# Optimization experiments

Measured on AMD Instinct MI355X. Metric: run time of the kernel, lower is better.

The kernel has to match this reference:

```python
import jax, jax.numpy as jnp
import numpy as np

B, S, D = 4, 2048, 1024
H = 16
HD = D // H  # 64


def setup_inputs() -> dict:
    key = jax.random.key(0)
    ks = jax.random.split(key, 9)
    sc = 1.0 / np.sqrt(D)
    return {
        "hidden_states": jax.random.normal(ks[0], (B, S, D), jnp.float32),
        "Wq": jax.random.normal(ks[1], (D, D), jnp.float32) * sc,
        "bq": jnp.zeros((D,), jnp.float32),
        "Wk": jax.random.normal(ks[2], (D, D), jnp.float32) * sc,
        "bk": jnp.zeros((D,), jnp.float32),
        "Wv": jax.random.normal(ks[3], (D, D), jnp.float32) * sc,
        "bv": jnp.zeros((D,), jnp.float32),
        "Wo": jax.random.normal(ks[4], (D, D), jnp.float32) * sc,
        "bo": jnp.zeros((D,), jnp.float32),
    }


def _rope_emb(seq_len, head_dim, dtype):
    # Faithful to torch buffer: emb = cat(sin(pos*inv_freq), cos(pos*inv_freq))
    inv_freq = 1.0 / (10000.0 ** (jnp.arange(0, head_dim, 2, dtype=jnp.float32) / head_dim))
    sinusoid = jnp.arange(seq_len, dtype=jnp.float32)[:, None] * inv_freq[None, :]  # [S, hd/2]
    return jnp.concatenate([jnp.sin(sinusoid), jnp.cos(sinusoid)], axis=-1).astype(dtype)  # [S, hd]


def _rotate(x, c, s):
    # x: [B,H,S,hd]; c,s: [1,1,S,hd/2]
    x1, x2 = x[..., : HD // 2], x[..., HD // 2 :]
    return jnp.concatenate([x1 * c - x2 * s, x2 * c + x1 * s], axis=-1)


def reference(hidden_states, Wq, bq, Wk, bk, Wv, bv, Wo, bo):
    b, s, d = hidden_states.shape

    def proj(W, bias):
        y = jnp.einsum("bsd,ed->bse", hidden_states, W) + bias
        return y.reshape(b, s, H, HD).transpose(0, 2, 1, 3)  # [B,H,S,hd]

    q, k, v = proj(Wq, bq), proj(Wk, bk), proj(Wv, bv)

    emb = _rope_emb(s, HD, hidden_states.dtype)
    # NOTE: original code names first half 'cos' though the buffer stores sin first.
    c = emb[None, None, :, : HD // 2]
    sn = emb[None, None, :, HD // 2 :]
    q = _rotate(q, c, sn)
    k = _rotate(k, c, sn)

    scores = jnp.einsum("bhqd,bhkd->bhqk", q, k) / jnp.sqrt(jnp.asarray(HD, hidden_states.dtype))
    probs = jax.nn.softmax(scores, axis=-1)
    ctx = jnp.einsum("bhqk,bhkd->bhqd", probs, v)
    ctx = ctx.transpose(0, 2, 1, 3).reshape(b, s, d)  # [B,S,D]
    return jnp.einsum("bsd,ed->bse", ctx, Wo) + bo
```

## Files before the change

### kernel.cpp

```cpp
#include <hip/hip_runtime.h>
#include <cmath>

#define B_ 4
#define S_ 2048
#define D_ 1024
#define H_ 16
#define HD_ 64

typedef __attribute__((ext_vector_type(8))) _Float16 half8;
typedef __attribute__((ext_vector_type(2))) _Float16 half2t;
typedef __attribute__((ext_vector_type(2))) __fp16 fp16x2;
typedef __attribute__((ext_vector_type(4))) float floatx4;
typedef __attribute__((ext_vector_type(16))) float floatx16;
typedef __attribute__((ext_vector_type(2))) unsigned uint2v;

union H2U { unsigned u; half2t h; fp16x2 f; };
__device__ __forceinline__ unsigned hpack2(float a, float b) {
    H2U x; x.h[0] = (_Float16)a; x.h[1] = (_Float16)b; return x.u;
}
__device__ __forceinline__ unsigned pkrtz(float a, float b) {
    H2U x; x.f = __builtin_amdgcn_cvt_pkrtz(a, b); return x.u;
}
__device__ __forceinline__ float h_lo(unsigned u) { H2U x; x.u = u; return (float)x.h[0]; }
__device__ __forceinline__ float h_hi(unsigned u) { H2U x; x.u = u; return (float)x.h[1]; }

__device__ __forceinline__ void barrier_lgkm() {
    asm volatile("s_waitcnt lgkmcnt(0)\n\ts_barrier" ::: "memory");
}

__global__ __launch_bounds__(256)
void conv_x(const float* __restrict__ x, unsigned short* __restrict__ o, int n)
{
    const int i = (blockIdx.x * 256 + threadIdx.x) * 8;
    if (i >= n) return;
    const float4 a = *(const float4*)(x + i);
    const float4 b = *(const float4*)(x + i + 4);
    *(uint4*)(o + i) = make_uint4(hpack2(a.x, a.y), hpack2(a.z, a.w),
                                  hpack2(b.x, b.y), hpack2(b.z, b.w));
}

__global__ __launch_bounds__(256)
void conv_weights(const float* __restrict__ Wq, const float* __restrict__ Wk,
                  const float* __restrict__ Wv, const float* __restrict__ Wo,
                  const float* __restrict__ bq, const float* __restrict__ bk,
                  const float* __restrict__ bv,
                  unsigned short* __restrict__ Wqkvf, unsigned short* __restrict__ Wof,
                  float* __restrict__ bqkv)
{
    const int bxx = blockIdx.x;
    const int t = threadIdx.x;
    if (bxx < 2048) {
        const int w = bxx >> 9;
        const int i = ((bxx & 511) * 256 + t) * 8;
        const float* src = (w == 0) ? Wq : (w == 1) ? Wk : (w == 2) ? Wv : Wo;
        const float4 a = *(const float4*)(src + i);
        const float4 b = *(const float4*)(src + i + 4);
        const uint4 v = make_uint4(hpack2(a.x, a.y), hpack2(a.z, a.w),
                                   hpack2(b.x, b.y), hpack2(b.z, b.w));
        if (w < 3)
            *(uint4*)(Wqkvf + (size_t)w * 1048576 + i) = v;
        else
            *(uint4*)(Wof + i) = v;
    } else {
        const int idx = t * 4;
        *(float4*)(bqkv + idx)        = *(const float4*)(bq + idx);
        *(float4*)(bqkv + 1024 + idx) = *(const float4*)(bk + idx);
        *(float4*)(bqkv + 2048 + idx) = *(const float4*)(bv + idx);
    }
}

template<int OBF>
__global__ __launch_bounds__(256, 2)
void gemm_half(const unsigned short* __restrict__ Ap, const unsigned short* __restrict__ Bp,
               const float* __restrict__ bias, void* __restrict__ Cout,
               int M, int N, int K)
{
    __shared__ uint4 ASH[512];
    __shared__ uint4 BSH[512];

    const int tid = threadIdx.x;
    const int bm = blockIdx.x * 128;
    const int bn = blockIdx.y * 128;
    const int w = tid >> 6, l = tid & 63;
    const int wm = (w & 1) * 64, wn = (w >> 1) * 64;

    floatx4 acc[4][4];
#pragma unroll
    for (int i = 0; i < 4; ++i)
#pragma unroll
        for (int j = 0; j < 4; ++j)
#pragma unroll
            for (int r = 0; r < 4; ++r) acc[i][j][r] = 0.f;

    const int r0 = tid >> 1, scb = (tid & 1) * 2;
    const size_t ga = (size_t)(bm + r0) * K + scb * 8;
    const size_t gb = (size_t)(bn + r0) * K + scb * 8;
    const int blk = r0 >> 4, r15 = r0 & 15;
    const int p1 = (scb << 4) + r15;
    const int f0a = (blk << 6) + (p1 ^ (scb << 1));
    const int f0b = (blk << 6) + ((p1 + 16) ^ ((scb + 1) << 1));

    const half8* pA = (const half8*)ASH;
    const half8* pB = (const half8*)BSH;
    const int lg = l ^ ((l >> 4) << 1);
    const int am = (wm >> 4) * 64 + lg;
    const int bnf = (wn >> 4) * 64 + lg;

    uint4 vA0 = *(const uint4*)(Ap + ga);
    uint4 vA1 = *(const uint4*)(Ap + ga + 8);
    uint4 vB0 = *(const uint4*)(Bp + gb);
    uint4 vB1 = *(const uint4*)(Bp + gb + 8);

    for (int k0 = 0; k0 < K; k0 += 32) {
        __syncthreads();
        ASH[f0a] = vA0; ASH[f0b] = vA1;
        BSH[f0a] = vB0; BSH[f0b] = vB1;
        __syncthreads();

        const int kn = (k0 + 32 < K) ? k0 + 32 : k0;
        vA0 = *(const uint4*)(Ap + ga + kn);
        vA1 = *(const uint4*)(Ap + ga + kn + 8);
        vB0 = *(const uint4*)(Bp + gb + kn);
        vB1 = *(const uint4*)(Bp + gb + kn + 8);

        half8 a[4];
#pragma unroll
        for (int i = 0; i < 4; ++i) a[i] = pA[am + i * 64];
#pragma unroll
        for (int j = 0; j < 4; ++j) {
            const half8 b = pB[bnf + j * 64];
#pragma unroll
            for (int i = 0; i < 4; ++i)
                acc[i][j] = __builtin_amdgcn_mfma_f32_16x16x32_f16(a[i], b, acc[i][j], 0, 0, 0);
        }
    }

    const int cr = (l >> 4) << 2;
    const int cc = l & 15;
#pragma unroll
    for (int j = 0; j < 4; ++j) {
        const int col = bn + wn + j * 16 + cc;
        const float bv = bias[col];
#pragma unroll
        for (int i = 0; i < 4; ++i) {
            const int row = bm + wm + i * 16 + cr;
#pragma unroll
            for (int r = 0; r < 4; ++r) {
                const float vv = acc[i][j][r] + bv;
                if (OBF) {
                    ((unsigned short*)Cout)[(size_t)(row + r) * N + col] =
                        (unsigned short)(hpack2(vv, vv) & 0xffffu);
                } else {
                    ((float*)Cout)[(size_t)(row + r) * N + col] = vv;
                }
            }
        }
    }
}

__global__ __launch_bounds__(256)
void prep_fused(const unsigned short* __restrict__ qkv,
                unsigned short* __restrict__ Qf, unsigned short* __restrict__ Kfo,
                unsigned short* __restrict__ Vt)
{
    __shared__ unsigned T[64][65];
    const int bx = blockIdx.x;
    const int t = threadIdx.x;
    if (bx < B_ * S_) {
        const int s = bx & (S_ - 1);
        const size_t rbase = (size_t)bx * 3072;
        const size_t obase = (size_t)bx * D_;
        const int h = t >> 4;
        const int i2 = (t & 15) * 2;
        const float kfreq = 0.28782313662425572f;
        const float KS = 0.18033688011112042f;

        const float f0 = expf(-(float)i2 * kfreq);
        const float f1 = expf(-(float)(i2 + 1) * kfreq);
        const float t0 = (float)s * f0, t1 = (float)s * f1;
        const float sn0 = sinf(t0), cs0 = cosf(t0);
        const float sn1 = sinf(t1), cs1 = cosf(t1);

        const size_t c1 = (size_t)h * 64 + i2;
        const size_t c2 = c1 + 32;

        const unsigned uq1 = *(const unsigned*)(qkv + rbase + c1);
        const unsigned uq2 = *(const unsigned*)(qkv + rbase + c2);
        const unsigned uk1 = *(const unsigned*)(qkv + rbase + 1024 + c1);
        const unsigned uk2 = *(const unsigned*)(qkv + rbase + 1024 + c2);
        const float q1x = h_lo(uq1), q1y = h_hi(uq1);
        const float q2x = h_lo(uq2), q2y = h_hi(uq2);
        const float k1x = h_lo(uk1), k1y = h_hi(uk1);
        const float k2x = h_lo(uk2), k2y = h_hi(uk2);

        *(unsigned*)(Qf + obase + c1) = hpack2(q1x * sn0 - q2x * cs0, q1y * sn1 - q2y * cs1);
        *(unsigned*)(Qf + obase + c2) = hpack2(q2x * sn0 + q1x * cs0, q2y * sn1 + q1y * cs1);
        *(unsigned*)(Kfo + obase + c1) = hpack2((k1x * sn0 - k2x * cs0) * KS, (k1y * sn1 - k2y * cs1) * KS);
        *(unsigned*)(Kfo + obase + c2) = hpack2((k2x * sn0 + k1x * cs0) * KS, (k2y * sn1 + k1y * cs1) * KS);
    } else {
        const int vb = bx - B_ * S_;
        const int st = vb & 31;
        const int h  = (vb >> 5) & 15;
        const int b  = vb >> 9;
        const int s0 = st * 64;
#pragma unroll
        for (int it = 0; it < 2; ++it) {
            const int idx = it * 256 + t;
            const int row = idx >> 3;
            const int c8 = (idx & 7) * 8;
            const uint4 u = *(const uint4*)(qkv + ((size_t)(b * S_ + s0 + row)) * 3072 + 2048 + h * 64 + c8);
            T[row][c8+0] = u.x & 0xffffu; T[row][c8+1] = u.x >> 16;
            T[row][c8+2] = u.y & 0xffffu; T[row][c8+3] = u.y >> 16;
            T[row][c8+4] = u.z & 0xffffu; T[row][c8+5] = u.z >> 16;
            T[row][c8+6] = u.w & 0xffffu; T[row][c8+7] = u.w >> 16;
        }
        __syncthreads();
        const int d = t >> 2;
        const int scg = (t & 3) * 16;
        unsigned u[8];
#pragma unroll
        for (int ii = 0; ii < 8; ++ii)
            u[ii] = T[scg + 2*ii][d] | (T[scg + 2*ii + 1][d] << 16);
        unsigned short* dst = Vt + ((size_t)((b * H_ + h) * 64 + d)) * S_ + s0 + scg;
        *(uint4*)(dst)     = make_uint4(u[0], u[1], u[2], u[3]);
        *(uint4*)(dst + 8) = make_uint4(u[4], u[5], u[6], u[7]);
    }
}

__global__ __launch_bounds__(256)
void attn_mfma32(const unsigned short* __restrict__ Qf,
                 const unsigned short* __restrict__ Kfi,
                 const unsigned short* __restrict__ Vt,
                 unsigned short* __restrict__ Cf)
{
    __shared__ uint4 KF[2][512];
    __shared__ uint4 VF[2][512];

    const int t = threadIdx.x;
    const int i = blockIdx.x;
    const int xcd = i & 7, j = i >> 3;
    const int bh = xcd * 8 + (j >> 4);
    const int qblk = j & 15;
    const int b = bh >> 4, h = bh & 15;

    const int w = t >> 6, l = t & 63;
    const int lq = l & 31, h5 = l >> 5;
    const int qrow = qblk * 128 + w * 32 + lq;

    half8 qf[4];
    const unsigned short* qp = Qf + ((size_t)(b * S_ + qrow)) * D_ + h * 64 + h5 * 8;
#pragma unroll
    for (int kc = 0; kc < 4; ++kc) qf[kc] = *(const half8*)(qp + kc * 16);

    floatx16 o0, o1, o2, z16;
#pragma unroll
    for (int r = 0; r < 16; ++r) { o0[r] = 0.f; o1[r] = 0.f; o2[r] = 0.f; z16[r] = 0.f; }

    union { unsigned u[4]; half8 s; } onesf;
    const unsigned ov = (lq == 0) ? 0x3C003C00u : 0u;
    onesf.u[0] = ov; onesf.u[1] = ov; onesf.u[2] = ov; onesf.u[3] = ov;

    const int sr = t >> 2, sc = t & 3;
    const unsigned short* gK0 = Kfi + ((size_t)(b * S_ + sr)) * D_ + h * 64 + sc * 16;
    const unsigned short* gV0 = Vt + ((size_t)((b * H_ + h) * 64 + sr)) * S_ + sc * 16;
    const int e0 = (sr >> 5) * 256 + sc * 64 + ((sr & 31) ^ (sc << 1));
    const int lx[4] = { l, l ^ 2, l ^ 4, l ^ 6 };

    const half8* pK = (const half8*)KF;
    const half8* pV = (const half8*)VF;
    (void)pK; (void)pV;

    uint4 ka  = *(const uint4*)(gK0);
    uint4 kb2 = *(const uint4*)(gK0 + 8);
    uint4 va  = *(const uint4*)(gV0);
    uint4 vb2 = *(const uint4*)(gV0 + 8);
    KF[0][e0] = ka; KF[0][e0 + 32] = kb2;
    VF[0][e0] = va; VF[0][e0 + 32] = vb2;
    {
        const unsigned short* gK = gK0 + (size_t)64 * D_;
        const unsigned short* gV = gV0 + 64;
        ka  = *(const uint4*)(gK);
        kb2 = *(const uint4*)(gK + 8);
        va  = *(const uint4*)(gV);
        vb2 = *(const uint4*)(gV + 8);
    }
    __syncthreads();

    for (int kt = 0; kt < 32; ++kt) {
        const int cur = kt & 1;

        if (kt < 31) {
            uint4* wK = KF[cur ^ 1];
            uint4* wV = VF[cur ^ 1];
            wK[e0] = ka; wK[e0 + 32] = kb2;
            wV[e0] = va; wV[e0 + 32] = vb2;
        }
        if (kt < 30) {
            const unsigned short* gK = gK0 + (size_t)(kt + 2) * 64 * D_;
            const unsigned short* gV = gV0 + (size_t)(kt + 2) * 64;
            ka  = *(const uint4*)(gK);
            kb2 = *(const uint4*)(gK + 8);
            va  = *(const uint4*)(gV);
            vb2 = *(const uint4*)(gV + 8);
        }

        const half8* pKc = (const half8*)KF[cur];
        const half8* pVc = (const half8*)VF[cur];

        __builtin_amdgcn_s_setprio(1);
        floatx16 st0 = __builtin_amdgcn_mfma_f32_32x32x16_f16(pKc[lx[0]],           qf[0], z16, 0, 0, 0);
        floatx16 st1 = __builtin_amdgcn_mfma_f32_32x32x16_f16(pKc[4 * 64 + lx[0]],  qf[0], z16, 0, 0, 0);
#pragma unroll
        for (int kc = 1; kc < 4; ++kc) {
            st0 = __builtin_amdgcn_mfma_f32_32x32x16_f16(pKc[kc * 64 + lx[kc]],       qf[kc], st0, 0, 0, 0);
            st1 = __builtin_amdgcn_mfma_f32_32x32x16_f16(pKc[(4 + kc) * 64 + lx[kc]], qf[kc], st1, 0, 0, 0);
        }
        __builtin_amdgcn_s_setprio(0);

        unsigned pu0[8], pu1[8];
#pragma unroll
        for (int g = 0; g < 8; ++g) {
            pu0[g] = pkrtz(__builtin_amdgcn_exp2f(st0[2 * g]),
                           __builtin_amdgcn_exp2f(st0[2 * g + 1]));
            pu1[g] = pkrtz(__builtin_amdgcn_exp2f(st1[2 * g]),
                           __builtin_amdgcn_exp2f(st1[2 * g + 1]));
        }

        __builtin_amdgcn_s_setprio(1);
#pragma unroll
        for (int kc = 0; kc < 4; ++kc) {
            const unsigned* pus = (kc >> 1) ? pu1 : pu0;
            const int g0 = (kc & 1) * 4;
            const uint2v r02 = __builtin_amdgcn_permlane32_swap(pus[g0 + 0], pus[g0 + 2], false, false);
            const uint2v r13 = __builtin_amdgcn_permlane32_swap(pus[g0 + 1], pus[g0 + 3], false, false);
            union { unsigned u[4]; half8 s; } pf;
            pf.u[0] = r02[0];
            pf.u[1] = r13[0];
            pf.u[2] = r02[1];
            pf.u[3] = r13[1];
            o0 = __builtin_amdgcn_mfma_f32_32x32x16_f16(pVc[kc * 64 + lx[kc]],       pf.s, o0, 0, 0, 0);
            o1 = __builtin_amdgcn_mfma_f32_32x32x16_f16(pVc[(4 + kc) * 64 + lx[kc]], pf.s, o1, 0, 0, 0);
            o2 = __builtin_amdgcn_mfma_f32_32x32x16_f16(onesf.s,                     pf.s, o2, 0, 0, 0);
        }
        __builtin_amdgcn_s_setprio(0);

        if (kt < 31) barrier_lgkm();
    }

    union { float f; unsigned u; } lc; lc.f = o2[0];
    const uint2v lr = __builtin_amdgcn_permlane32_swap(lc.u, lc.u, false, false);
    union { unsigned u; float f; } ls; ls.u = lr[0];
    const float inv = 1.0f / ls.f;

    const size_t cbase = ((size_t)(b * S_ + qrow)) * D_ + h * 64;
#pragma unroll
    for (int rq = 0; rq < 4; ++rq) {
        const int d0 = rq * 8 + h5 * 4;
        const uint2 y0 = make_uint2(hpack2(o0[4*rq+0] * inv, o0[4*rq+1] * inv),
                                    hpack2(o0[4*rq+2] * inv, o0[4*rq+3] * inv));
        const uint2 y1 = make_uint2(hpack2(o1[4*rq+0] * inv, o1[4*rq+1] * inv),
                                    hpack2(o1[4*rq+2] * inv, o1[4*rq+3] * inv));
        *(uint2*)(Cf + cbase + d0)      = y0;
        *(uint2*)(Cf + cbase + 32 + d0) = y1;
    }
}

extern "C" void kernel_launch(void* const* d_in, const int* in_sizes, int n_in,
                              void* d_out, int out_size, void* d_ws, size_t ws_size,
                              hipStream_t stream) {
    (void)in_sizes; (void)n_in; (void)out_size; (void)ws_size;
    const float* X  = (const float*)d_in[0];
    const float* Wq = (const float*)d_in[1];
    const float* bq = (const float*)d_in[2];
    const float* Wk = (const float*)d_in[3];
    const float* bk = (const float*)d_in[4];
    const float* Wv = (const float*)d_in[5];
    const float* bv = (const float*)d_in[6];
    const float* Wo = (const float*)d_in[7];
    const float* bo = (const float*)d_in[8];
    float* out = (float*)d_out;

    char* ws = (char*)d_ws;
#define OFF(mb) (ws + ((size_t)(mb) << 20))
    unsigned short* Xf    = (unsigned short*)OFF(0);
    unsigned short* qkv16 = (unsigned short*)OFF(16);
    unsigned short* Qf    = (unsigned short*)OFF(64);
    unsigned short* Kfb   = (unsigned short*)OFF(80);
    unsigned short* Vtb   = (unsigned short*)OFF(96);
    unsigned short* Wqkvf = (unsigned short*)OFF(112);
    unsigned short* Wof   = (unsigned short*)OFF(118);
    float*          bqkv  = (float*)OFF(120);
    unsigned short* Cf    = (unsigned short*)OFF(0);
#undef OFF

    const int NX = B_ * S_ * D_;
    conv_x<<<NX / 2048, 256, 0, stream>>>(X, Xf, NX);
    conv_weights<<<2049, 256, 0, stream>>>(Wq, Wk, Wv, Wo, bq, bk, bv,
                                           Wqkvf, Wof, bqkv);
    gemm_half<1><<<dim3(64, 24), 256, 0, stream>>>(Xf, Wqkvf, bqkv,
                                                   qkv16, B_*S_, 3 * D_, D_);
    prep_fused<<<B_*S_ + 2048, 256, 0, stream>>>(qkv16, Qf, Kfb, Vtb);
    attn_mfma32<<<1024, 256, 0, stream>>>(Qf, Kfb, Vtb, Cf);
    gemm_half<0><<<dim3(64, 8), 256, 0, stream>>>(Cf, Wof, bo, out, B_*S_, D_, D_);
}
```

Measured before the change: 306.6 us.

## Software-pipeline PV MFMAs one tile behind QK and triple-buffer V

Restructures the attention loop so the P·V MFMAs for tile kt-1 run after the QK and exp work of tile kt, which lets the exp/convert phase overlap with matrix work. V shared memory goes from double to triple buffering to hold the lagging tile, and a drain step handles the last tile after the loop. It also adds a launch-bounds occupancy hint of 4 blocks per CU. The costs are more registers for the carried P fragments, more LDS, and possible spilling under the new launch bound.

```diff
diff --git a/kernel.cpp b/kernel.cpp
--- a/kernel.cpp
+++ b/kernel.cpp
@@ -227,14 +227,14 @@
     }
 }
 
-__global__ __launch_bounds__(256)
+__global__ __launch_bounds__(256, 4)
 void attn_mfma32(const unsigned short* __restrict__ Qf,
                  const unsigned short* __restrict__ Kfi,
                  const unsigned short* __restrict__ Vt,
                  unsigned short* __restrict__ Cf)
 {
     __shared__ uint4 KF[2][512];
-    __shared__ uint4 VF[2][512];
+    __shared__ uint4 VF[3][512];
 
     const int t = threadIdx.x;
     const int i = blockIdx.x;
@@ -265,10 +265,6 @@
     const unsigned short* gV0 = Vt + ((size_t)((b * H_ + h) * 64 + sr)) * S_ + sc * 16;
     const int e0 = (sr >> 5) * 256 + sc * 64 + ((sr & 31) ^ (sc << 1));
     const int lx[4] = { l, l ^ 2, l ^ 4, l ^ 6 };
-
-    const half8* pK = (const half8*)KF;
-    const half8* pV = (const half8*)VF;
-    (void)pK; (void)pV;
 
     uint4 ka  = *(const uint4*)(gK0);
     uint4 kb2 = *(const uint4*)(gK0 + 8);
@@ -286,12 +282,13 @@
     }
     __syncthreads();
 
+    unsigned pfr[4][4];
+    int vm1 = 2, vcur = 0, vp1 = 1;
+
     for (int kt = 0; kt < 32; ++kt) {
-        const int cur = kt & 1;
-
         if (kt < 31) {
-            uint4* wK = KF[cur ^ 1];
-            uint4* wV = VF[cur ^ 1];
+            uint4* wK = KF[(kt + 1) & 1];
+            uint4* wV = VF[vp1];
             wK[e0] = ka; wK[e0 + 32] = kb2;
             wV[e0] = va; wV[e0 + 32] = vb2;
         }
@@ -304,8 +301,7 @@
             vb2 = *(const uint4*)(gV + 8);
         }
 
-        const half8* pKc = (const half8*)KF[cur];
-        const half8* pVc = (const half8*)VF[cur];
+        const half8* pKc = (const half8*)KF[kt & 1];
 
         __builtin_amdgcn_s_setprio(1);
         floatx16 st0 = __builtin_amdgcn_mfma_f32_32x32x16_f16(pKc[lx[0]],           qf[0], z16, 0, 0, 0);
@@ -326,25 +322,49 @@
                            __builtin_amdgcn_exp2f(st1[2 * g + 1]));
         }
 
-        __builtin_amdgcn_s_setprio(1);
+        if (kt > 0) {
+            const half8* pVc = (const half8*)VF[vm1];
+            __builtin_amdgcn_s_setprio(1);
+#pragma unroll
+            for (int kc = 0; kc < 4; ++kc) {
+                union { unsigned u[4]; half8 s; } pfs;
+                pfs.u[0] = pfr[kc][0]; pfs.u[1] = pfr[kc][1];
+                pfs.u[2] = pfr[kc][2]; pfs.u[3] = pfr[kc][3];
+                o0 = __builtin_amdgcn_mfma_f32_32x32x16_f16(pVc[kc * 64 + lx[kc]],       pfs.s, o0, 0, 0, 0);
+                o1 = __builtin_amdgcn_mfma_f32_32x32x16_f16(pVc[(4 + kc) * 64 + lx[kc]], pfs.s, o1, 0, 0, 0);
+                o2 = __builtin_amdgcn_mfma_f32_32x32x16_f16(onesf.s,                     pfs.s, o2, 0, 0, 0);
+            }
+            __builtin_amdgcn_s_setprio(0);
+        }
+
 #pragma unroll
         for (int kc = 0; kc < 4; ++kc) {
             const unsigned* pus = (kc >> 1) ? pu1 : pu0;
             const int g0 = (kc & 1) * 4;
             const uint2v r02 = __builtin_amdgcn_permlane32_swap(pus[g0 + 0], pus[g0 + 2], false, false);
             const uint2v r13 = __builtin_amdgcn_permlane32_swap(pus[g0 + 1], pus[g0 + 3], false, false);
-            union { unsigned u[4]; half8 s; } pf;
-            pf.u[0] = r02[0];
-            pf.u[1] = r13[0];
-            pf.u[2] = r02[1];
-            pf.u[3] = r13[1];
-            o0 = __builtin_amdgcn_mfma_f32_32x32x16_f16(pVc[kc * 64 + lx[kc]],       pf.s, o0, 0, 0, 0);
-            o1 = __builtin_amdgcn_mfma_f32_32x32x16_f16(pVc[(4 + kc) * 64 + lx[kc]], pf.s, o1, 0, 0, 0);
-            o2 = __builtin_amdgcn_mfma_f32_32x32x16_f16(onesf.s,                     pf.s, o2, 0, 0, 0);
-        }
-        __builtin_amdgcn_s_setprio(0);
+            pfr[kc][0] = r02[0];
+            pfr[kc][1] = r13[0];
+            pfr[kc][2] = r02[1];
+            pfr[kc][3] = r13[1];
+        }
+
+        { const int tmp = vm1; vm1 = vcur; vcur = vp1; vp1 = tmp; }
 
         if (kt < 31) barrier_lgkm();
+    }
+
+    {
+        const half8* pVc = (const half8*)VF[vm1];
+#pragma unroll
+        for (int kc = 0; kc < 4; ++kc) {
+            union { unsigned u[4]; half8 s; } pfs;
+            pfs.u[0] = pfr[kc][0]; pfs.u[1] = pfr[kc][1];
+            pfs.u[2] = pfr[kc][2]; pfs.u[3] = pfr[kc][3];
+            o0 = __builtin_amdgcn_mfma_f32_32x32x16_f16(pVc[kc * 64 + lx[kc]],       pfs.s, o0, 0, 0, 0);
+            o1 = __builtin_amdgcn_mfma_f32_32x32x16_f16(pVc[(4 + kc) * 64 + lx[kc]], pfs.s, o1, 0, 0, 0);
+            o2 = __builtin_amdgcn_mfma_f32_32x32x16_f16(onesf.s,                     pfs.s, o2, 0, 0, 0);
+        }
     }
 
     union { float f; unsigned u; } lc; lc.f = o2[0];
```

Measured after the change: 405.3 us. +32.2%, slower.

## Fuse RoPE into QKV GEMM epilogue and merge conversion kernels

Applied to the files above, without the earlier changes.

The QKV projection GEMM now applies the rotary embedding and the K scaling in its epilogue and writes Q and K straight to their final buffers. Only V goes to a temporary buffer, which a smaller transpose kernel then reads. The input and weight fp32-to-fp16 conversion kernels are merged into one launch. This drops the full qkv intermediate round trip and one launch, but the epilogue now computes sin/cos per element, which adds transcendental work inside the GEMM.

```diff
diff --git a/kernel.cpp b/kernel.cpp
--- a/kernel.cpp
+++ b/kernel.cpp
@@ -29,26 +29,25 @@
 }
 
 __global__ __launch_bounds__(256)
-void conv_x(const float* __restrict__ x, unsigned short* __restrict__ o, int n)
+void conv_all(const float* __restrict__ x, unsigned short* __restrict__ o,
+              const float* __restrict__ Wq, const float* __restrict__ Wk,
+              const float* __restrict__ Wv, const float* __restrict__ Wo,
+              const float* __restrict__ bq, const float* __restrict__ bk,
+              const float* __restrict__ bv,
+              unsigned short* __restrict__ Wqkvf, unsigned short* __restrict__ Wof,
+              float* __restrict__ bqkv)
 {
-    const int i = (blockIdx.x * 256 + threadIdx.x) * 8;
-    if (i >= n) return;
-    const float4 a = *(const float4*)(x + i);
-    const float4 b = *(const float4*)(x + i + 4);
-    *(uint4*)(o + i) = make_uint4(hpack2(a.x, a.y), hpack2(a.z, a.w),
-                                  hpack2(b.x, b.y), hpack2(b.z, b.w));
-}
-
-__global__ __launch_bounds__(256)
-void conv_weights(const float* __restrict__ Wq, const float* __restrict__ Wk,
-                  const float* __restrict__ Wv, const float* __restrict__ Wo,
-                  const float* __restrict__ bq, const float* __restrict__ bk,
-                  const float* __restrict__ bv,
-                  unsigned short* __restrict__ Wqkvf, unsigned short* __restrict__ Wof,
-                  float* __restrict__ bqkv)
-{
-    const int bxx = blockIdx.x;
     const int t = threadIdx.x;
+    const int bx = blockIdx.x;
+    if (bx < 4096) {
+        const int i = (bx * 256 + t) * 8;
+        const float4 a = *(const float4*)(x + i);
+        const float4 b = *(const float4*)(x + i + 4);
+        *(uint4*)(o + i) = make_uint4(hpack2(a.x, a.y), hpack2(a.z, a.w),
+                                      hpack2(b.x, b.y), hpack2(b.z, b.w));
+        return;
+    }
+    const int bxx = bx - 4096;
     if (bxx < 2048) {
         const int w = bxx >> 9;
         const int i = ((bxx & 511) * 256 + t) * 8;
@@ -69,10 +68,11 @@
     }
 }
 
-template<int OBF>
+template<int MODE>
 __global__ __launch_bounds__(256, 2)
 void gemm_half(const unsigned short* __restrict__ Ap, const unsigned short* __restrict__ Bp,
-               const float* __restrict__ bias, void* __restrict__ Cout,
+               const float* __restrict__ bias, void* __restrict__ C0,
+               void* __restrict__ C1, void* __restrict__ C2,
                int M, int N, int K)
 {
     __shared__ uint4 ASH[512];
@@ -137,94 +137,105 @@
 
     const int cr = (l >> 4) << 2;
     const int cc = l & 15;
-#pragma unroll
-    for (int j = 0; j < 4; ++j) {
-        const int col = bn + wn + j * 16 + cc;
-        const float bv = bias[col];
-#pragma unroll
-        for (int i = 0; i < 4; ++i) {
-            const int row = bm + wm + i * 16 + cr;
-#pragma unroll
-            for (int r = 0; r < 4; ++r) {
-                const float vv = acc[i][j][r] + bv;
-                if (OBF) {
-                    ((unsigned short*)Cout)[(size_t)(row + r) * N + col] =
-                        (unsigned short)(hpack2(vv, vv) & 0xffffu);
-                } else {
-                    ((float*)Cout)[(size_t)(row + r) * N + col] = vv;
+
+    if (MODE == 0) {
+#pragma unroll
+        for (int j = 0; j < 4; ++j) {
+            const int col = bn + wn + j * 16 + cc;
+            const float bv = bias[col];
+#pragma unroll
+            for (int i = 0; i < 4; ++i) {
+                const int row = bm + wm + i * 16 + cr;
+#pragma unroll
+                for (int r = 0; r < 4; ++r) {
+                    ((float*)C0)[(size_t)(row + r) * N + col] = acc[i][j][r] + bv;
                 }
             }
         }
+    } else {
+        const int reg = bn >> 10;
+        if (reg < 2) {
+            const float KSs = (reg == 1) ? 0.18033688011112042f : 1.0f;
+            unsigned short* dst0 = (unsigned short*)((reg == 0) ? C0 : C1);
+            const int hbase = (bn - (reg << 10)) + wn;
+            const float kfreq = 0.28782313662425572f;
+#pragma unroll
+            for (int j = 0; j < 2; ++j) {
+                const int d = j * 16 + cc;
+                const float fd = expf(-(float)d * kfreq);
+                const float b1 = bias[bn + wn + j * 16 + cc];
+                const float b2 = bias[bn + wn + j * 16 + cc + 32];
+#pragma unroll
+                for (int i = 0; i < 4; ++i) {
+                    const int row0 = bm + wm + i * 16 + cr;
+#pragma unroll
+                    for (int r = 0; r < 4; ++r) {
+                        const int row = row0 + r;
+                        const int s = row & (S_ - 1);
+                        const float tt = (float)s * fd;
+                        const float sn = sinf(tt), cs = cosf(tt);
+                        const float x1 = acc[i][j][r] + b1;
+                        const float x2 = acc[i][j + 2][r] + b2;
+                        const float o1 = (x1 * sn - x2 * cs) * KSs;
+                        const float o2 = (x2 * sn + x1 * cs) * KSs;
+                        unsigned short* p = dst0 + (size_t)row * D_ + hbase + d;
+                        p[0]  = (unsigned short)(hpack2(o1, o1) & 0xffffu);
+                        p[32] = (unsigned short)(hpack2(o2, o2) & 0xffffu);
+                    }
+                }
+            }
+        } else {
+#pragma unroll
+            for (int j = 0; j < 4; ++j) {
+                const int col = bn + wn + j * 16 + cc;
+                const float bv = bias[col];
+                const int vcol = col - 2048;
+#pragma unroll
+                for (int i = 0; i < 4; ++i) {
+                    const int row0 = bm + wm + i * 16 + cr;
+#pragma unroll
+                    for (int r = 0; r < 4; ++r) {
+                        const float vv = acc[i][j][r] + bv;
+                        ((unsigned short*)C2)[(size_t)(row0 + r) * 1024 + vcol] =
+                            (unsigned short)(hpack2(vv, vv) & 0xffffu);
+                    }
+                }
+            }
+        }
     }
 }
 
 __global__ __launch_bounds__(256)
-void prep_fused(const unsigned short* __restrict__ qkv,
-                unsigned short* __restrict__ Qf, unsigned short* __restrict__ Kfo,
-                unsigned short* __restrict__ Vt)
+void prep_v(const unsigned short* __restrict__ Vtmp, unsigned short* __restrict__ Vt)
 {
     __shared__ unsigned T[64][65];
-    const int bx = blockIdx.x;
+    const int vb = blockIdx.x;
     const int t = threadIdx.x;
-    if (bx < B_ * S_) {
-        const int s = bx & (S_ - 1);
-        const size_t rbase = (size_t)bx * 3072;
-        const size_t obase = (size_t)bx * D_;
-        const int h = t >> 4;
-        const int i2 = (t & 15) * 2;
-        const float kfreq = 0.28782313662425572f;
-        const float KS = 0.18033688011112042f;
-
-        const float f0 = expf(-(float)i2 * kfreq);
-        const float f1 = expf(-(float)(i2 + 1) * kfreq);
-        const float t0 = (float)s * f0, t1 = (float)s * f1;
-        const float sn0 = sinf(t0), cs0 = cosf(t0);
-        const float sn1 = sinf(t1), cs1 = cosf(t1);
-
-        const size_t c1 = (size_t)h * 64 + i2;
-        const size_t c2 = c1 + 32;
-
-        const unsigned uq1 = *(const unsigned*)(qkv + rbase + c1);
-        const unsigned uq2 = *(const unsigned*)(qkv + rbase + c2);
-        const unsigned uk1 = *(const unsigned*)(qkv + rbase + 1024 + c1);
-        const unsigned uk2 = *(const unsigned*)(qkv + rbase + 1024 + c2);
-        const float q1x = h_lo(uq1), q1y = h_hi(uq1);
-        const float q2x = h_lo(uq2), q2y = h_hi(uq2);
-        const float k1x = h_lo(uk1), k1y = h_hi(uk1);
-        const float k2x = h_lo(uk2), k2y = h_hi(uk2);
-
-        *(unsigned*)(Qf + obase + c1) = hpack2(q1x * sn0 - q2x * cs0, q1y * sn1 - q2y * cs1);
-        *(unsigned*)(Qf + obase + c2) = hpack2(q2x * sn0 + q1x * cs0, q2y * sn1 + q1y * cs1);
-        *(unsigned*)(Kfo + obase + c1) = hpack2((k1x * sn0 - k2x * cs0) * KS, (k1y * sn1 - k2y * cs1) * KS);
-        *(unsigned*)(Kfo + obase + c2) = hpack2((k2x * sn0 + k1x * cs0) * KS, (k2y * sn1 + k1y * cs1) * KS);
-    } else {
-        const int vb = bx - B_ * S_;
-        const int st = vb & 31;
-        const int h  = (vb >> 5) & 15;
-        const int b  = vb >> 9;
-        const int s0 = st * 64;
-#pragma unroll
-        for (int it = 0; it < 2; ++it) {
-            const int idx = it * 256 + t;
-            const int row = idx >> 3;
-            const int c8 = (idx & 7) * 8;
-            const uint4 u = *(const uint4*)(qkv + ((size_t)(b * S_ + s0 + row)) * 3072 + 2048 + h * 64 + c8);
-            T[row][c8+0] = u.x & 0xffffu; T[row][c8+1] = u.x >> 16;
-            T[row][c8+2] = u.y & 0xffffu; T[row][c8+3] = u.y >> 16;
-            T[row][c8+4] = u.z & 0xffffu; T[row][c8+5] = u.z >> 16;
-            T[row][c8+6] = u.w & 0xffffu; T[row][c8+7] = u.w >> 16;
-        }
-        __syncthreads();
-        const int d = t >> 2;
-        const int scg = (t & 3) * 16;
-        unsigned u[8];
-#pragma unroll
-        for (int ii = 0; ii < 8; ++ii)
-            u[ii] = T[scg + 2*ii][d] | (T[scg + 2*ii + 1][d] << 16);
-        unsigned short* dst = Vt + ((size_t)((b * H_ + h) * 64 + d)) * S_ + s0 + scg;
-        *(uint4*)(dst)     = make_uint4(u[0], u[1], u[2], u[3]);
-        *(uint4*)(dst + 8) = make_uint4(u[4], u[5], u[6], u[7]);
-    }
+    const int st = vb & 31;
+    const int h  = (vb >> 5) & 15;
+    const int b  = vb >> 9;
+    const int s0 = st * 64;
+#pragma unroll
+    for (int it = 0; it < 2; ++it) {
+        const int idx = it * 256 + t;
+        const int row = idx >> 3;
+        const int c8 = (idx & 7) * 8;
+        const uint4 u = *(const uint4*)(Vtmp + ((size_t)(b * S_ + s0 + row)) * 1024 + h * 64 + c8);
+        T[row][c8+0] = u.x & 0xffffu; T[row][c8+1] = u.x >> 16;
+        T[row][c8+2] = u.y & 0xffffu; T[row][c8+3] = u.y >> 16;
+        T[row][c8+4] = u.z & 0xffffu; T[row][c8+5] = u.z >> 16;
+        T[row][c8+6] = u.w & 0xffffu; T[row][c8+7] = u.w >> 16;
+    }
+    __syncthreads();
+    const int d = t >> 2;
+    const int scg = (t & 3) * 16;
+    unsigned u[8];
+#pragma unroll
+    for (int ii = 0; ii < 8; ++ii)
+        u[ii] = T[scg + 2*ii][d] | (T[scg + 2*ii + 1][d] << 16);
+    unsigned short* dst = Vt + ((size_t)((b * H_ + h) * 64 + d)) * S_ + s0 + scg;
+    *(uint4*)(dst)     = make_uint4(u[0], u[1], u[2], u[3]);
+    *(uint4*)(dst + 8) = make_uint4(u[4], u[5], u[6], u[7]);
 }
 
 __global__ __launch_bounds__(256)
@@ -265,10 +276,6 @@
     const unsigned short* gV0 = Vt + ((size_t)((b * H_ + h) * 64 + sr)) * S_ + sc * 16;
     const int e0 = (sr >> 5) * 256 + sc * 64 + ((sr & 31) ^ (sc << 1));
     const int lx[4] = { l, l ^ 2, l ^ 4, l ^ 6 };
-
-    const half8* pK = (const half8*)KF;
-    const half8* pV = (const half8*)VF;
-    (void)pK; (void)pV;
 
     uint4 ka  = *(const uint4*)(gK0);
     uint4 kb2 = *(const uint4*)(gK0 + 8);
@@ -383,7 +390,7 @@
     char* ws = (char*)d_ws;
 #define OFF(mb) (ws + ((size_t)(mb) << 20))
     unsigned short* Xf    = (unsigned short*)OFF(0);
-    unsigned short* qkv16 = (unsigned short*)OFF(16);
+    unsigned short* Vtmp  = (unsigned short*)OFF(16);
     unsigned short* Qf    = (unsigned short*)OFF(64);
     unsigned short* Kfb   = (unsigned short*)OFF(80);
     unsigned short* Vtb   = (unsigned short*)OFF(96);
@@ -393,13 +400,12 @@
     unsigned short* Cf    = (unsigned short*)OFF(0);
 #undef OFF
 
-    const int NX = B_ * S_ * D_;
-    conv_x<<<NX / 2048, 256, 0, stream>>>(X, Xf, NX);
-    conv_weights<<<2049, 256, 0, stream>>>(Wq, Wk, Wv, Wo, bq, bk, bv,
-                                           Wqkvf, Wof, bqkv);
+    conv_all<<<6145, 256, 0, stream>>>(X, Xf, Wq, Wk, Wv, Wo, bq, bk, bv,
+                                       Wqkvf, Wof, bqkv);
     gemm_half<1><<<dim3(64, 24), 256, 0, stream>>>(Xf, Wqkvf, bqkv,
-                                                   qkv16, B_*S_, 3 * D_, D_);
-    prep_fused<<<B_*S_ + 2048, 256, 0, stream>>>(qkv16, Qf, Kfb, Vtb);
+                                                   Qf, Kfb, Vtmp, B_*S_, 3 * D_, D_);
+    prep_v<<<2048, 256, 0, stream>>>(Vtmp, Vtb);
     attn_mfma32<<<1024, 256, 0, stream>>>(Qf, Kfb, Vtb, Cf);
-    gemm_half<0><<<dim3(64, 8), 256, 0, stream>>>(Cf, Wof, bo, out, B_*S_, D_, D_);
-}
+    gemm_half<0><<<dim3(64, 8), 256, 0, stream>>>(Cf, Wof, bo, out, nullptr, nullptr,
+                                                  B_*S_, D_, D_);
+}
```

Result: slower. 672.4 us (+119.3%).
